# Optimization experiments

Hardware: AMD Instinct MI355X
Metric: run time of the kernel (lower is better)

## Reference

```python
import jax, jax.numpy as jnp
import numpy as np


def setup_inputs() -> dict:
    key = jax.random.key(0)
    k1, k2 = jax.random.split(key)
    B, F = 512, 1024
    K, D = 100, 5
    inputs = jax.random.normal(k1, (B, F), dtype=jnp.float32)
    T = jax.random.normal(k2, (F, K * D), dtype=jnp.float32) * 0.05  # random_normal init
    return {"inputs": inputs, "T": T}


def reference(inputs, T):
    NUM_KERNELS, DIM_PER_KERNEL = 100, 5
    B = inputs.shape[0]
    # project: [B, F] @ [F, K*D] -> [B, K, D]
    x = (inputs @ T).reshape(B, NUM_KERNELS, DIM_PER_KERNEL)
    # pairwise L1 over D: abs_diffs[i, k, j] = sum_d |x[i,k,d] - x[j,k,d]|
    # diffs: [B, K, D, B]
    diffs = x[:, :, :, None] - jnp.transpose(x, (1, 2, 0))[None, :, :, :]
    abs_diffs = jnp.sum(jnp.abs(diffs), axis=2)  # [B, K, B]
    # sum over other-batch axis (includes self term exp(0)=1, as in original)
    minibatch_features = jnp.sum(jnp.exp(-abs_diffs), axis=2)  # [B, K]
    return minibatch_features
```

## Files before the change

### kernel.cpp

```cpp
#include <hip/hip_runtime.h>


#define BB 512
#define FF 1024
#define KK 100
#define KD 500
#define KDP 512
#define SPLITS 8
#define FN (FF / SPLITS)
#define STEPS (FN / 16)
#define LOG2E 1.4426950408889634f

__global__ __launch_bounds__(256, 2) void kA(
    const float* __restrict__ in, const float* __restrict__ T,
    float* __restrict__ xpT)
{
    __shared__ __align__(16) float smem[2112];
    float (*Ads)[68] = (float(*)[68])smem;
    float (*Bds)[64] = (float(*)[64])(smem + 1088);

    const int b = blockIdx.x;
    const int t = threadIdx.x;
    const int i0  = (b & 7) * 64;
    const int kd0 = ((b >> 3) & 7) * 64;
    const int s   = b >> 6;
    const int tk  = t & 15;
    const int ti  = t >> 4;

    float acc[4][4];
    #pragma unroll
    for (int r = 0; r < 4; ++r)
        #pragma unroll
        for (int c = 0; c < 4; ++c) acc[r][c] = 0.f;

    const int ia  = t >> 2;
    const int fqa = t & 3;
    const int kb  = t & 63;
    const int frb = t >> 6;
    const int kbc = min(kd0 + kb, KD - 1);

    const float* inb = in + (size_t)(i0 + ia) * FF + s * FN;
    const float* Tb  = T + (size_t)(s * FN) * KD + kbc;

    float4 av = *(const float4*)&inb[fqa * 4];
    float bv0 = Tb[(size_t)(frb * 4 + 0) * KD];
    float bv1 = Tb[(size_t)(frb * 4 + 1) * KD];
    float bv2 = Tb[(size_t)(frb * 4 + 2) * KD];
    float bv3 = Tb[(size_t)(frb * 4 + 3) * KD];

    for (int step = 0; step < STEPS; ++step) {
        Ads[fqa * 4 + 0][ia] = av.x;
        Ads[fqa * 4 + 1][ia] = av.y;
        Ads[fqa * 4 + 2][ia] = av.z;
        Ads[fqa * 4 + 3][ia] = av.w;
        Bds[frb * 4 + 0][kb] = bv0;
        Bds[frb * 4 + 1][kb] = bv1;
        Bds[frb * 4 + 2][kb] = bv2;
        Bds[frb * 4 + 3][kb] = bv3;
        __syncthreads();

        if (step + 1 < STEPS) {
            const int fo = (step + 1) * 16;
            av  = *(const float4*)&inb[fo + fqa * 4];
            bv0 = Tb[(size_t)(fo + frb * 4 + 0) * KD];
            bv1 = Tb[(size_t)(fo + frb * 4 + 1) * KD];
            bv2 = Tb[(size_t)(fo + frb * 4 + 2) * KD];
            bv3 = Tb[(size_t)(fo + frb * 4 + 3) * KD];
        }

        #pragma unroll
        for (int f = 0; f < 16; ++f) {
            float4 a  = *(const float4*)&Ads[f][ti * 4];
            float4 bq = *(const float4*)&Bds[f][tk * 4];
            float ar[4] = {a.x, a.y, a.z, a.w};
            float br[4] = {bq.x, bq.y, bq.z, bq.w};
            #pragma unroll
            for (int r = 0; r < 4; ++r)
                #pragma unroll
                for (int c = 0; c < 4; ++c)
                    acc[r][c] = fmaf(ar[r], br[c], acc[r][c]);
        }
        __syncthreads();
    }

    #pragma unroll
    for (int c = 0; c < 4; ++c) {
        float4 v = {acc[0][c], acc[1][c], acc[2][c], acc[3][c]};
        *(float4*)&xpT[((size_t)s * KDP + kd0 + tk * 4 + c) * BB + i0 + ti * 4] = v;
    }
}

__global__ __launch_bounds__(512) void pairf(
    const float* __restrict__ xpT, float* __restrict__ out)
{
    const int k = blockIdx.x;
    const int p = blockIdx.y;
    const int t = threadIdx.x;
    const int lane = t & 63;
    const int w    = t >> 6;

    __shared__ float xs[BB][8];
    __shared__ float ps[8][128];

    #pragma unroll
    for (int d = 0; d < 5; ++d) {
        float v = 0.f;
        #pragma unroll
        for (int s = 0; s < SPLITS; ++s)
            v += xpT[((size_t)s * KDP + k * 5 + d) * BB + t];
        xs[t][d] = LOG2E * v;
    }
    __syncthreads();

    const int ia = p * 128 + lane;
    float xa[5], xb[5];
    #pragma unroll
    for (int d = 0; d < 5; ++d) { xa[d] = xs[ia][d]; xb[d] = xs[ia + 64][d]; }

    float sa = 0.f, sb = 0.f;
    const int j0 = w << 6;
    #pragma unroll 2
    for (int jj = 0; jj < 64; ++jj) {
        const int j = j0 + jj;
        float4 xj0 = *(const float4*)&xs[j][0];
        float  xj4 = xs[j][4];
        float aa = (fabsf(xa[0] - xj0.x) + fabsf(xa[1] - xj0.y))
                 + (fabsf(xa[2] - xj0.z) + fabsf(xa[3] - xj0.w))
                 + fabsf(xa[4] - xj4);
        float bb = (fabsf(xb[0] - xj0.x) + fabsf(xb[1] - xj0.y))
                 + (fabsf(xb[2] - xj0.z) + fabsf(xb[3] - xj0.w))
                 + fabsf(xb[4] - xj4);
        sa += __builtin_amdgcn_exp2f(-aa);
        sb += __builtin_amdgcn_exp2f(-bb);
    }

    ps[w][lane]      = sa;
    ps[w][lane + 64] = sb;
    __syncthreads();

    if (t < 128) {
        float v = 0.f;
        #pragma unroll
        for (int q = 0; q < 8; ++q) v += ps[q][t];
        out[(size_t)(p * 128 + t) * KK + k] = v;
    }
}

__global__ __launch_bounds__(1024, 1) void mbd_fused(
    const float* __restrict__ in, const float* __restrict__ T, float* __restrict__ out)
{
    const int k = blockIdx.x;
    const int t = threadIdx.x;
    const int i = t & (BB - 1);
    const int h = t >> 9;

    __shared__ float xk[1024][8];

    float a0 = 0.f, a1 = 0.f, a2 = 0.f, a3 = 0.f, a4 = 0.f;
    const float4* inrow = (const float4*)(in + (size_t)i * FF + (size_t)h * 512);
    const float* Tk = T + 5 * k + (size_t)h * 512 * KD;

    for (int ff = 0; ff < 512; ff += 4) {
        float4 v = inrow[ff >> 2];
        const float* tp = Tk + (size_t)ff * KD;
        a0 = fmaf(v.x, tp[0], a0); a1 = fmaf(v.x, tp[1], a1); a2 = fmaf(v.x, tp[2], a2);
        a3 = fmaf(v.x, tp[3], a3); a4 = fmaf(v.x, tp[4], a4); tp += KD;
        a0 = fmaf(v.y, tp[0], a0); a1 = fmaf(v.y, tp[1], a1); a2 = fmaf(v.y, tp[2], a2);
        a3 = fmaf(v.y, tp[3], a3); a4 = fmaf(v.y, tp[4], a4); tp += KD;
        a0 = fmaf(v.z, tp[0], a0); a1 = fmaf(v.z, tp[1], a1); a2 = fmaf(v.z, tp[2], a2);
        a3 = fmaf(v.z, tp[3], a3); a4 = fmaf(v.z, tp[4], a4); tp += KD;
        a0 = fmaf(v.w, tp[0], a0); a1 = fmaf(v.w, tp[1], a1); a2 = fmaf(v.w, tp[2], a2);
        a3 = fmaf(v.w, tp[3], a3); a4 = fmaf(v.w, tp[4], a4);
    }
    xk[t][0] = a0; xk[t][1] = a1; xk[t][2] = a2; xk[t][3] = a3; xk[t][4] = a4;
    __syncthreads();
    if (t < BB) {
        xk[t][0] += xk[t + BB][0]; xk[t][1] += xk[t + BB][1]; xk[t][2] += xk[t + BB][2];
        xk[t][3] += xk[t + BB][3]; xk[t][4] += xk[t + BB][4];
    }
    __syncthreads();

    const int jg = t >> 9;
    const float4 xiv = *(const float4*)&xk[i][0];
    const float xi4 = xk[i][4];
    float s0 = 0.f;
    const int j0 = jg << 8;
    for (int jj = 0; jj < 256; ++jj) {
        const int j = j0 + jj;
        float4 xj = *(const float4*)&xk[j][0];
        float xj4 = xk[j][4];
        float aa = (fabsf(xiv.x - xj.x) + fabsf(xiv.y - xj.y))
                 + (fabsf(xiv.z - xj.z) + fabsf(xiv.w - xj.w)) + fabsf(xi4 - xj4);
        s0 += __builtin_amdgcn_exp2f(-1.4426950408889634f * aa);
    }
    xk[BB + i][jg] = s0;
    __syncthreads();
    if (t < BB)
        out[(size_t)t * KK + k] = xk[BB + t][0] + xk[BB + t][1];
}

extern "C" void kernel_launch(void* const* d_in, const int* in_sizes, int n_in,
                              void* d_out, int out_size, void* d_ws, size_t ws_size,
                              hipStream_t stream) {
    const float* in = (const float*)d_in[0];
    const float* T  = (const float*)d_in[1];
    float* out = (float*)d_out;

    const size_t xpT_bytes = (size_t)SPLITS * KDP * BB * sizeof(float);

    if (ws_size < xpT_bytes) {
        mbd_fused<<<KK, 1024, 0, stream>>>(in, T, out);
        return;
    }

    float* xpT = (float*)d_ws;

    kA<<<512, 256, 0, stream>>>(in, T, xpT);

    dim3 g2(KK, 4);
    pairf<<<g2, 512, 0, stream>>>(xpT, out);
}
```

Before: 35.18 us.

## Split-K reduce into separate kernel and tile pairwise stage over j with atomics

Moves the split-K partial-sum reduction and log2e scaling out of the pairwise kernel into a new elementwise kernel that writes a reduced transposed x. The pairwise kernel now also tiles over the j (other-batch) axis, launching 1600 smaller blocks of 256 threads instead of 400 blocks of 512. Partial sums are combined with atomic adds into an output cleared by a memset. This adds an extra kernel launch, a memset, and float atomics, which make the summation order nondeterministic.

After: 40.83 us. 16.1% more time.

```diff
diff --git a/kernel.cpp b/kernel.cpp
--- a/kernel.cpp
+++ b/kernel.cpp
@@ -90,59 +90,89 @@
     }
 }
 
-__global__ __launch_bounds__(512) void pairf(
-    const float* __restrict__ xpT, float* __restrict__ out)
-{
-    const int k = blockIdx.x;
-    const int p = blockIdx.y;
-    const int t = threadIdx.x;
+__global__ __launch_bounds__(256) void kB(
+    const float* __restrict__ xpT, float* __restrict__ xT)
+{
+    const int e = blockIdx.x * 256 + threadIdx.x;
+    const float4* p = (const float4*)xpT;
+    float4 v = p[e];
+    #pragma unroll
+    for (int s = 1; s < SPLITS; ++s) {
+        float4 w = p[(size_t)s * (KDP * BB / 4) + e];
+        v.x += w.x; v.y += w.y; v.z += w.z; v.w += w.w;
+    }
+    v.x *= LOG2E; v.y *= LOG2E; v.z *= LOG2E; v.w *= LOG2E;
+    ((float4*)xT)[e] = v;
+}
+
+__global__ __launch_bounds__(256) void pairZ(
+    const float* __restrict__ xT, float* __restrict__ out)
+{
+    const int k  = blockIdx.x;
+    const int ip = blockIdx.y;
+    const int jp = blockIdx.z;
+    const int t  = threadIdx.x;
     const int lane = t & 63;
     const int w    = t >> 6;
 
-    __shared__ float xs[BB][8];
-    __shared__ float ps[8][128];
-
+    __shared__ float xs4[128][4];
+    __shared__ float xs1[128];
+    __shared__ float ps[4][128];
+
+    for (int e = t; e < 640; e += 256) {
+        const int d  = e >> 7;
+        const int jj = e & 127;
+        const float v = xT[(size_t)(k * 5 + d) * BB + jp * 128 + jj];
+        if (d < 4) xs4[jj][d] = v; else xs1[jj] = v;
+    }
+    __syncthreads();
+
+    float xa[5], xb[5];
     #pragma unroll
     for (int d = 0; d < 5; ++d) {
-        float v = 0.f;
-        #pragma unroll
-        for (int s = 0; s < SPLITS; ++s)
-            v += xpT[((size_t)s * KDP + k * 5 + d) * BB + t];
-        xs[t][d] = LOG2E * v;
-    }
-    __syncthreads();
-
-    const int ia = p * 128 + lane;
-    float xa[5], xb[5];
-    #pragma unroll
-    for (int d = 0; d < 5; ++d) { xa[d] = xs[ia][d]; xb[d] = xs[ia + 64][d]; }
-
-    float sa = 0.f, sb = 0.f;
-    const int j0 = w << 6;
+        xa[d] = xT[(size_t)(k * 5 + d) * BB + ip * 128 + lane];
+        xb[d] = xT[(size_t)(k * 5 + d) * BB + ip * 128 + 64 + lane];
+    }
+
+    float sa0 = 0.f, sa1 = 0.f, sb0 = 0.f, sb1 = 0.f;
+    const int j0 = w << 5;
     #pragma unroll 2
-    for (int jj = 0; jj < 64; ++jj) {
-        const int j = j0 + jj;
-        float4 xj0 = *(const float4*)&xs[j][0];
-        float  xj4 = xs[j][4];
-        float aa = (fabsf(xa[0] - xj0.x) + fabsf(xa[1] - xj0.y))
-                 + (fabsf(xa[2] - xj0.z) + fabsf(xa[3] - xj0.w))
-                 + fabsf(xa[4] - xj4);
-        float bb = (fabsf(xb[0] - xj0.x) + fabsf(xb[1] - xj0.y))
-                 + (fabsf(xb[2] - xj0.z) + fabsf(xb[3] - xj0.w))
-                 + fabsf(xb[4] - xj4);
-        sa += __builtin_amdgcn_exp2f(-aa);
-        sb += __builtin_amdgcn_exp2f(-bb);
-    }
-
-    ps[w][lane]      = sa;
-    ps[w][lane + 64] = sb;
+    for (int jj = 0; jj < 32; jj += 2) {
+        {
+            const int j = j0 + jj;
+            float4 xj = *(const float4*)&xs4[j][0];
+            float  x4 = xs1[j];
+            float aa = (fabsf(xa[0] - xj.x) + fabsf(xa[1] - xj.y))
+                     + (fabsf(xa[2] - xj.z) + fabsf(xa[3] - xj.w))
+                     + fabsf(xa[4] - x4);
+            float bb = (fabsf(xb[0] - xj.x) + fabsf(xb[1] - xj.y))
+                     + (fabsf(xb[2] - xj.z) + fabsf(xb[3] - xj.w))
+                     + fabsf(xb[4] - x4);
+            sa0 += __builtin_amdgcn_exp2f(-aa);
+            sb0 += __builtin_amdgcn_exp2f(-bb);
+        }
+        {
+            const int j = j0 + jj + 1;
+            float4 xj = *(const float4*)&xs4[j][0];
+            float  x4 = xs1[j];
+            float aa = (fabsf(xa[0] - xj.x) + fabsf(xa[1] - xj.y))
+                     + (fabsf(xa[2] - xj.z) + fabsf(xa[3] - xj.w))
+                     + fabsf(xa[4] - x4);
+            float bb = (fabsf(xb[0] - xj.x) + fabsf(xb[1] - xj.y))
+                     + (fabsf(xb[2] - xj.z) + fabsf(xb[3] - xj.w))
+                     + fabsf(xb[4] - x4);
+            sa1 += __builtin_amdgcn_exp2f(-aa);
+            sb1 += __builtin_amdgcn_exp2f(-bb);
+        }
+    }
+
+    ps[w][lane]      = sa0 + sa1;
+    ps[w][lane + 64] = sb0 + sb1;
     __syncthreads();
 
     if (t < 128) {
-        float v = 0.f;
-        #pragma unroll
-        for (int q = 0; q < 8; ++q) v += ps[q][t];
-        out[(size_t)(p * 128 + t) * KK + k] = v;
+        const float v = (ps[0][t] + ps[1][t]) + (ps[2][t] + ps[3][t]);
+        unsafeAtomicAdd(&out[(size_t)(ip * 128 + t) * KK + k], v);
     }
 }
 
@@ -207,16 +237,21 @@
     float* out = (float*)d_out;
 
     const size_t xpT_bytes = (size_t)SPLITS * KDP * BB * sizeof(float);
-
-    if (ws_size < xpT_bytes) {
+    const size_t xT_bytes  = (size_t)KDP * BB * sizeof(float);
+
+    if (ws_size < xpT_bytes + xT_bytes) {
         mbd_fused<<<KK, 1024, 0, stream>>>(in, T, out);
         return;
     }
 
     float* xpT = (float*)d_ws;
+    float* xT  = (float*)((char*)d_ws + xpT_bytes);
+
+    hipMemsetAsync(out, 0, (size_t)BB * KK * sizeof(float), stream);
 
     kA<<<512, 256, 0, stream>>>(in, T, xpT);
-
-    dim3 g2(KK, 4);
-    pairf<<<g2, 512, 0, stream>>>(xpT, out);
-}
+    kB<<<256, 256, 0, stream>>>(xpT, xT);
+
+    dim3 g3(KK, 4, 4);
+    pairZ<<<g3, 256, 0, stream>>>(xT, out);
+}
```
